# Optimization experiments

Hardware: AMD Instinct MI355X
Metric: run time of the kernel (lower is better)

The kernel has to match this reference:

```python
import jax, jax.numpy as jnp
import numpy as np

N = 100000
E = 800000
D_IN = 128
D_H = 128
D_OUT = 40
L = 16
ALPHA = 0.1
THETA = 0.5
BN_EPS = 1e-5


def setup_inputs() -> dict:
    key = jax.random.key(0)
    ks = jax.random.split(key, 8)
    x = jax.random.normal(ks[0], (N, D_IN), dtype=jnp.float32)
    edge_row = jax.random.randint(ks[1], (E,), 0, N, dtype=jnp.int32)
    edge_col = jax.random.randint(ks[2], (E,), 0, N, dtype=jnp.int32)
    edge_weight = jax.random.uniform(ks[3], (E,), dtype=jnp.float32) / 8.0  # ~normalized adj values
    W_in = jax.random.normal(ks[4], (D_IN, D_H), dtype=jnp.float32) / np.sqrt(D_IN)
    b_in = jnp.zeros((D_H,), jnp.float32)
    conv_W = jax.random.normal(ks[5], (L, D_H, D_H), dtype=jnp.float32) / np.sqrt(D_H)
    bn_gamma = jnp.ones((L, D_H), jnp.float32)
    bn_beta = jnp.zeros((L, D_H), jnp.float32)
    W_out = jax.random.normal(ks[6], (D_H, D_OUT), dtype=jnp.float32) / np.sqrt(D_H)
    b_out = jnp.zeros((D_OUT,), jnp.float32)
    return {"x": x, "edge_weight": edge_weight, "W_in": W_in, "b_in": b_in,
            "conv_W": conv_W, "bn_gamma": bn_gamma, "bn_beta": bn_beta,
            "W_out": W_out, "b_out": b_out,
            "edge_row": edge_row, "edge_col": edge_col}


def reference(x, edge_weight, W_in, b_in, conv_W, bn_gamma, bn_beta, W_out, b_out, edge_row, edge_col):
    # input linear + relu (dropout p=0 -> identity)
    x0 = jax.nn.relu(x @ W_in + b_in)            # [N, D_H]
    # GCN2Conv beta coefficients: log(theta/layer + 1), layer = 1..L
    betas = jnp.log(THETA / jnp.arange(1, L + 1, dtype=jnp.float32) + 1.0)

    def spmm(h):
        # out[i] = sum_{e: row[e]=i} w[e] * h[col[e]]
        msgs = edge_weight[:, None] * h[edge_col]     # [E, D_H]
        return jax.ops.segment_sum(msgs, edge_row, num_segments=N)

    def layer(h, params):
        W, g, bb, beta = params
        a = spmm(h)                                   # propagate
        a = (1.0 - ALPHA) * a + ALPHA * x0            # initial-residual mix
        a = (1.0 - beta) * a + beta * (a @ W)         # shared-weights identity mapping
        mu = jnp.mean(a, axis=0)                      # BatchNorm1d (training stats)
        var = jnp.var(a, axis=0)
        a = (a - mu) * jax.lax.rsqrt(var + BN_EPS) * g + bb
        a = a + h                                     # residual
        return jax.nn.relu(a), None

    xL, _ = jax.lax.scan(layer, x0, (conv_W, bn_gamma, bn_beta, betas))
    return xL @ W_out + b_out                         # [N, D_OUT]
```

## Files before the change

### kernel.cpp

```cpp
#include <hip/hip_runtime.h>
#include <math.h>

#define NN 100000
#define EE 800000
#define DH 128
#define NL 16
#define GEMM_GRID 1563
#define SG_GRID 782
#define NSLOT 32

typedef __bf16 bf16x8 __attribute__((ext_vector_type(8)));
typedef float f32x4 __attribute__((ext_vector_type(4)));

__global__ void k_hist(const int* __restrict__ row, int* __restrict__ cnt) {
    int e = blockIdx.x * 256 + threadIdx.x;
    if (e < EE) atomicAdd(&cnt[row[e]], 1);
}

__global__ void k_scan1(const int* __restrict__ cnt, int* __restrict__ rp, int* __restrict__ part) {
    __shared__ int buf[512];
    int tid = threadIdx.x;
    int i = blockIdx.x * 512 + tid;
    int v = (i < NN) ? cnt[i] : 0;
    buf[tid] = v;
    __syncthreads();
    for (int off = 1; off < 512; off <<= 1) {
        int x = (tid >= off) ? buf[tid - off] : 0;
        __syncthreads();
        buf[tid] += x;
        __syncthreads();
    }
    if (i < NN) rp[i] = buf[tid] - v;
    if (tid == 511) part[blockIdx.x] = buf[511];
}

__global__ void k_scan2(int* __restrict__ part, int nparts) {
    __shared__ int buf[256];
    int tid = threadIdx.x;
    int v = (tid < nparts) ? part[tid] : 0;
    buf[tid] = v;
    __syncthreads();
    for (int off = 1; off < 256; off <<= 1) {
        int x = (tid >= off) ? buf[tid - off] : 0;
        __syncthreads();
        buf[tid] += x;
        __syncthreads();
    }
    if (tid < nparts) part[tid] = buf[tid] - v;
}

__global__ void k_scan3(int* __restrict__ rp, const int* __restrict__ part) {
    int i = blockIdx.x * 512 + threadIdx.x;
    if (i < NN) rp[i] += part[blockIdx.x];
    if (i == 0) rp[NN] = EE;
}

__global__ void k_fill(const int* __restrict__ row, const int* __restrict__ col,
                       const float* __restrict__ w, const int* __restrict__ rp,
                       int* __restrict__ fil, int2* __restrict__ ep) {
    int e = blockIdx.x * 256 + threadIdx.x;
    if (e >= EE) return;
    int r = row[e];
    int pos = rp[r] + atomicAdd(&fil[r], 1);
    ep[pos] = make_int2(col[e], __float_as_int(0.9f * w[e]));
}

__global__ void k_prep_w(const float* __restrict__ convW, const float* __restrict__ Win,
                         __bf16* __restrict__ Bhi, __bf16* __restrict__ Blo) {
    int l = blockIdx.x;
    const float* W;
    float beta, ob;
    if (l < NL) {
        beta = logf(0.5f / (float)(l + 1) + 1.0f);
        ob = 1.0f - beta;
        W = convW + (size_t)l * DH * DH;
    } else {
        beta = 1.0f;
        ob = 0.0f;
        W = Win;
    }
    __bf16* bh = Bhi + (size_t)l * DH * DH;
    __bf16* bl = Blo + (size_t)l * DH * DH;
    for (int i = threadIdx.x; i < DH * DH; i += 256) {
        int k = i >> 7, j = i & 127;
        float v = beta * W[i] + ((k == j) ? ob : 0.f);
        __bf16 hv = (__bf16)v;
        int t = j >> 4, n = j & 15, ks = k >> 5, quad = (k >> 3) & 3, e = k & 7;
        int off = ((t * 4 + ks) * 64 + quad * 16 + n) * 8 + e;
        bh[off] = hv;
        bl[off] = (__bf16)(v - (float)hv);
    }
}

__global__ void k_prep_out(const float* __restrict__ Wout, __bf16* __restrict__ Bhi, __bf16* __restrict__ Blo) {
    for (int i = threadIdx.x; i < DH * 48; i += 256) {
        int k = i / 48, j = i % 48;
        float v = (j < 40) ? Wout[k * 40 + j] : 0.f;
        __bf16 hv = (__bf16)v;
        int t = j >> 4, n = j & 15, ks = k >> 5, quad = (k >> 3) & 3, e = k & 7;
        int off = ((t * 4 + ks) * 64 + quad * 16 + n) * 8 + e;
        Bhi[off] = hv;
        Blo[off] = (__bf16)(v - (float)hv);
    }
}

__device__ inline void split8(const float* p, bf16x8& hi, bf16x8& lo) {
    f32x4 v0 = *(const f32x4*)p;
    f32x4 v1 = *(const f32x4*)(p + 4);
#pragma unroll
    for (int j = 0; j < 4; ++j) {
        __bf16 h0 = (__bf16)v0[j];
        hi[j] = h0;
        lo[j] = (__bf16)(v0[j] - (float)h0);
        __bf16 h1 = (__bf16)v1[j];
        hi[4 + j] = h1;
        lo[4 + j] = (__bf16)(v1[j] - (float)h1);
    }
}

#define MFMA(a, b, c) __builtin_amdgcn_mfma_f32_16x16x32_bf16(a, b, c, 0, 0, 0)

__device__ inline float dec_scale(unsigned int sc4, int ks) {
    return __uint_as_float(((sc4 >> (8 * ks)) & 0xffu) << 23);
}

#define DEC_DW(dw, wsv, a0, a1, a2, a3)                         \
    {                                                           \
        a0 = fmaf(wsv, (float)((dw)&0xffu), a0);                \
        a1 = fmaf(wsv, (float)(((dw) >> 8) & 0xffu), a1);       \
        a2 = fmaf(wsv, (float)(((dw) >> 16) & 0xffu), a2);      \
        a3 = fmaf(wsv, (float)((dw) >> 24), a3);                \
    }

#define EDGE_FMA(S4, W, RA, RB)                                       \
    {                                                                 \
        float _w = (W);                                               \
        float _w0 = _w * dec_scale(S4, 0);                            \
        float _w1 = _w * dec_scale(S4, 1);                            \
        float _w2 = _w * dec_scale(S4, 2);                            \
        float _w3 = _w * dec_scale(S4, 3);                            \
        sw0 += _w0; sw1 += _w1; sw2 += _w2; sw3 += _w3;               \
        DEC_DW((RA).x, _w0, acc[0][0], acc[0][1], acc[0][2], acc[0][3]); \
        DEC_DW((RA).y, _w0, acc[0][4], acc[0][5], acc[0][6], acc[0][7]); \
        DEC_DW((RA).z, _w1, acc[1][0], acc[1][1], acc[1][2], acc[1][3]); \
        DEC_DW((RA).w, _w1, acc[1][4], acc[1][5], acc[1][6], acc[1][7]); \
        DEC_DW((RB).x, _w2, acc[2][0], acc[2][1], acc[2][2], acc[2][3]); \
        DEC_DW((RB).y, _w2, acc[2][4], acc[2][5], acc[2][6], acc[2][7]); \
        DEC_DW((RB).z, _w3, acc[3][0], acc[3][1], acc[3][2], acc[3][3]); \
        DEC_DW((RB).w, _w3, acc[3][4], acc[3][5], acc[3][6], acc[3][7]); \
    }

__global__ void k_cvt8(const __bf16* __restrict__ src, unsigned char* __restrict__ q8,
                       unsigned char* __restrict__ sc) {
    int t = blockIdx.x * 256 + threadIdx.x;
    if (t >= NN * 4) return;
    int node = t >> 2, ks = t & 3;
    const __bf16* p = src + (size_t)node * DH + ks * 32;
    float v[32];
    float mx = 0.f;
#pragma unroll
    for (int i = 0; i < 4; ++i) {
        bf16x8 b = *(const bf16x8*)(p + i * 8);
#pragma unroll
        for (int c = 0; c < 8; ++c) {
            float f = (float)b[c];
            v[i * 8 + c] = f;
            mx = fmaxf(mx, fabsf(f));
        }
    }
    unsigned int em = (__float_as_uint(mx) >> 23) & 0xffu;
    unsigned int eb;
    float sinv;
    if (em < 7) { eb = 0; sinv = 0.f; }
    else { eb = em - 6; sinv = __uint_as_float((254 - eb) << 23); }
    sc[(size_t)node * 4 + ks] = (unsigned char)eb;
    unsigned char* bp = q8 + (size_t)node * 128 + (ks >> 1) * 64 + (ks & 1) * 8;
#pragma unroll
    for (int q = 0; q < 4; ++q) {
        uint2 w;
        w.x = 0; w.y = 0;
#pragma unroll
        for (int c = 0; c < 4; ++c) {
            unsigned int q0 = (unsigned int)rintf(fminf(fmaf(v[q * 8 + c], sinv, 128.f), 255.f));
            unsigned int q1 = (unsigned int)rintf(fminf(fmaf(v[q * 8 + 4 + c], sinv, 128.f), 255.f));
            w.x |= q0 << (8 * c);
            w.y |= q1 << (8 * c);
        }
        *(uint2*)(bp + q * 16) = w;
    }
}

__global__ __launch_bounds__(512, 4) void k_spmm_gemm(const unsigned char* __restrict__ hin8,
                                                      const unsigned char* __restrict__ hinsc,
                                                      const unsigned char* __restrict__ x08,
                                                      const unsigned char* __restrict__ x0sc,
                                                      const int* __restrict__ rp, const int2* __restrict__ ep,
                                                      __bf16* __restrict__ aout,
                                                      const __bf16* __restrict__ Bhi, const __bf16* __restrict__ Blo,
                                                      float* __restrict__ stats32) {
    __shared__ __bf16 Bs[2 * DH * DH];
    __shared__ float red[2][8][DH];
    int tid = threadIdx.x;
    {
        const f32x4* sh = (const f32x4*)Bhi;
        const f32x4* sl = (const f32x4*)Blo;
        f32x4* dh = (f32x4*)Bs;
        f32x4* dl = (f32x4*)(Bs + DH * DH);
#pragma unroll
        for (int i = 0; i < 4; ++i) {
            dh[tid + i * 512] = sh[tid + i * 512];
            dl[tid + i * 512] = sl[tid + i * 512];
        }
    }

    int wave = tid >> 6, lane = tid & 63;
    int n = lane & 15, quad = lane >> 4;
    int r0 = blockIdx.x * 128 + wave * 16;
    int node = r0 + n;
    int nc = (node < NN) ? node : (NN - 1);

    float acc[4][8];
#pragma unroll
    for (int ks = 0; ks < 4; ++ks)
#pragma unroll
        for (int c = 0; c < 8; ++c) acc[ks][c] = 0.f;
    float sw0 = 0.f, sw1 = 0.f, sw2 = 0.f, sw3 = 0.f;

    unsigned xs4 = *(const unsigned*)&x0sc[(size_t)nc * 4];
    const unsigned char* xb = x08 + (size_t)nc * 128 + quad * 16;
    uint4 xa = *(const uint4*)xb;
    uint4 xc = *(const uint4*)(xb + 64);

    int s = 0, e = 0;
    if (node < NN) { s = rp[node]; e = rp[node + 1]; }
    int cnt = e - s;
    int npairs = cnt >> 1;

    const unsigned char* hb = hin8 + quad * 16;

    int2 cP0, cP1, fP0, fP1;
    unsigned cS0, cS1;
    uint4 cA0, cB0, cA1, cB1;
    if (npairs > 0) {
        cP0 = ep[s]; cP1 = ep[s + 1];
        cS0 = *(const unsigned*)&hinsc[(size_t)cP0.x * 4];
        cS1 = *(const unsigned*)&hinsc[(size_t)cP1.x * 4];
        const unsigned char* b0 = hb + (size_t)cP0.x * 128;
        const unsigned char* b1 = hb + (size_t)cP1.x * 128;
        cA0 = *(const uint4*)b0; cB0 = *(const uint4*)(b0 + 64);
        cA1 = *(const uint4*)b1; cB1 = *(const uint4*)(b1 + 64);
        int jf = s + 2; if (jf > EE - 2) jf = EE - 2;
        fP0 = ep[jf]; fP1 = ep[jf + 1];
    }

    EDGE_FMA(xs4, 0.1f, xa, xc);

    int j = s;
    for (int it = 0; it < npairs; ++it) {
        int j2 = j + 4; if (j2 > EE - 2) j2 = EE - 2;
        int2 eN0 = ep[j2], eN1 = ep[j2 + 1];
        unsigned tS0 = *(const unsigned*)&hinsc[(size_t)fP0.x * 4];
        unsigned tS1 = *(const unsigned*)&hinsc[(size_t)fP1.x * 4];
        const unsigned char* b0 = hb + (size_t)fP0.x * 128;
        const unsigned char* b1 = hb + (size_t)fP1.x * 128;
        uint4 tA0 = *(const uint4*)b0, tB0 = *(const uint4*)(b0 + 64);
        uint4 tA1 = *(const uint4*)b1, tB1 = *(const uint4*)(b1 + 64);
        EDGE_FMA(cS0, __int_as_float(cP0.y), cA0, cB0);
        EDGE_FMA(cS1, __int_as_float(cP1.y), cA1, cB1);
        cP0 = fP0; cP1 = fP1; fP0 = eN0; fP1 = eN1;
        cS0 = tS0; cS1 = tS1;
        cA0 = tA0; cB0 = tB0; cA1 = tA1; cB1 = tB1;
        j += 2;
    }
    if (cnt & 1) {
        int2 pe = ep[e - 1];
        unsigned s4 = *(const unsigned*)&hinsc[(size_t)pe.x * 4];
        const unsigned char* bp = hb + (size_t)pe.x * 128;
        uint4 ra = *(const uint4*)bp, rb = *(const uint4*)(bp + 64);
        EDGE_FMA(s4, __int_as_float(pe.y), ra, rb);
    }

    bf16x8 av[4];
    {
        float sws[4] = {sw0, sw1, sw2, sw3};
#pragma unroll
        for (int ks = 0; ks < 4; ++ks)
#pragma unroll
            for (int c = 0; c < 8; ++c)
                av[ks][c] = (__bf16)(acc[ks][c] - 128.0f * sws[ks]);
    }

    __syncthreads();

    f32x4 gacc[8];
#pragma unroll
    for (int t = 0; t < 8; ++t) gacc[t] = (f32x4){0.f, 0.f, 0.f, 0.f};

#pragma unroll
    for (int ks = 0; ks < 4; ++ks) {
#pragma unroll
        for (int t = 0; t < 8; ++t) {
            int base = ((t * 4 + ks) * 64 + lane) * 8;
            bf16x8 bh = *(const bf16x8*)&Bs[base];
            bf16x8 bl = *(const bf16x8*)&Bs[DH * DH + base];
            gacc[t] = MFMA(av[ks], bh, gacc[t]);
            gacc[t] = MFMA(av[ks], bl, gacc[t]);
        }
    }

#pragma unroll
    for (int t = 0; t < 8; ++t) {
        float sm = 0.f, qq = 0.f;
#pragma unroll
        for (int r = 0; r < 4; ++r) {
            int row = r0 + quad * 4 + r;
            float v = gacc[t][r];
            if (row < NN) {
                aout[(size_t)row * DH + t * 16 + n] = (__bf16)v;
                sm += v;
                qq += v * v;
            }
        }
        sm += __shfl_xor(sm, 16); sm += __shfl_xor(sm, 32);
        qq += __shfl_xor(qq, 16); qq += __shfl_xor(qq, 32);
        if (quad == 0) {
            red[0][wave][t * 16 + n] = sm;
            red[1][wave][t * 16 + n] = qq;
        }
    }
    __syncthreads();
    if (tid < 256) {
        int which = tid >> 7, jj = tid & 127;
        float tot = 0.f;
#pragma unroll
        for (int w = 0; w < 8; ++w) tot += red[which][w][jj];
        atomicAdd(&stats32[(size_t)(blockIdx.x & (NSLOT - 1)) * 256 + tid], tot);
    }
}

__global__ __launch_bounds__(256) void k_lin_in(const float* __restrict__ X,
                                                const __bf16* __restrict__ Bhi, const __bf16* __restrict__ Blo,
                                                const float* __restrict__ bin, __bf16* __restrict__ x0) {
    __shared__ __bf16 Bs[2 * DH * DH];
    int tid = threadIdx.x;
    {
        const f32x4* sh = (const f32x4*)Bhi;
        const f32x4* sl = (const f32x4*)Blo;
        f32x4* dh = (f32x4*)Bs;
        f32x4* dl = (f32x4*)(Bs + DH * DH);
#pragma unroll
        for (int i = 0; i < 8; ++i) {
            dh[tid + i * 256] = sh[tid + i * 256];
            dl[tid + i * 256] = sl[tid + i * 256];
        }
    }
    __syncthreads();

    int wave = tid >> 6, lane = tid & 63;
    int n = lane & 15, quad = lane >> 4;
    int r0 = blockIdx.x * 64 + wave * 16;
    int arow = r0 + n;
    if (arow > NN - 1) arow = NN - 1;
    const float* pa = X + (size_t)arow * DH + quad * 8;

    f32x4 acc[8];
#pragma unroll
    for (int t = 0; t < 8; ++t) acc[t] = (f32x4){0.f, 0.f, 0.f, 0.f};

#pragma unroll
    for (int ks = 0; ks < 4; ++ks) {
        bf16x8 ah, al;
        split8(pa + ks * 32, ah, al);
#pragma unroll
        for (int t = 0; t < 8; ++t) {
            int base = ((t * 4 + ks) * 64 + lane) * 8;
            bf16x8 bh = *(const bf16x8*)&Bs[base];
            bf16x8 bl = *(const bf16x8*)&Bs[DH * DH + base];
            acc[t] = MFMA(ah, bh, acc[t]);
            acc[t] = MFMA(al, bh, acc[t]);
            acc[t] = MFMA(ah, bl, acc[t]);
        }
    }

#pragma unroll
    for (int t = 0; t < 8; ++t) {
        float bj = bin[t * 16 + n];
#pragma unroll
        for (int r = 0; r < 4; ++r) {
            int row = r0 + quad * 4 + r;
            if (row < NN) {
                float v = fmaxf(acc[t][r] + bj, 0.f);
                x0[(size_t)row * DH + t * 16 + n] = (__bf16)v;
            }
        }
    }
}

__global__ __launch_bounds__(256) void k_gemm_out(const __bf16* __restrict__ A,
                                                  const __bf16* __restrict__ Bhi, const __bf16* __restrict__ Blo,
                                                  const float* __restrict__ bout, float* __restrict__ out) {
    __shared__ __bf16 Bs[2 * 48 * DH];
    int tid = threadIdx.x;
    {
        const f32x4* sh = (const f32x4*)Bhi;
        const f32x4* sl = (const f32x4*)Blo;
        f32x4* dh = (f32x4*)Bs;
        f32x4* dl = (f32x4*)(Bs + 48 * DH);
#pragma unroll
        for (int i = 0; i < 3; ++i) {
            dh[tid + i * 256] = sh[tid + i * 256];
            dl[tid + i * 256] = sl[tid + i * 256];
        }
    }
    __syncthreads();

    int wave = tid >> 6, lane = tid & 63;
    int n = lane & 15, quad = lane >> 4;
    int r0 = blockIdx.x * 64 + wave * 16;
    int arow = r0 + n;
    if (arow > NN - 1) arow = NN - 1;
    const __bf16* pa = A + (size_t)arow * DH + quad * 8;

    f32x4 acc[3];
#pragma unroll
    for (int t = 0; t < 3; ++t) acc[t] = (f32x4){0.f, 0.f, 0.f, 0.f};

#pragma unroll
    for (int ks = 0; ks < 4; ++ks) {
        bf16x8 av = *(const bf16x8*)(pa + ks * 32);
#pragma unroll
        for (int t = 0; t < 3; ++t) {
            int base = ((t * 4 + ks) * 64 + lane) * 8;
            bf16x8 bh = *(const bf16x8*)&Bs[base];
            bf16x8 bl = *(const bf16x8*)&Bs[48 * DH + base];
            acc[t] = MFMA(av, bh, acc[t]);
            acc[t] = MFMA(av, bl, acc[t]);
        }
    }

#pragma unroll
    for (int t = 0; t < 3; ++t) {
        int j = t * 16 + n;
        float bj = (j < 40) ? bout[j] : 0.f;
#pragma unroll
        for (int r = 0; r < 4; ++r) {
            int row = r0 + quad * 4 + r;
            if (row < NN && j < 40) out[(size_t)row * 40 + j] = acc[t][r] + bj;
        }
    }
}

__global__ __launch_bounds__(256) void k_update(const __bf16* __restrict__ a, const __bf16* __restrict__ hin,
                                                __bf16* __restrict__ hout,
                                                unsigned char* __restrict__ h8, unsigned char* __restrict__ hsc,
                                                const float* __restrict__ stats32,
                                                const float* __restrict__ gamma, const float* __restrict__ bbeta) {
    __shared__ float scb[DH], shb[DH];
    int tid = threadIdx.x;
    if (tid < DH) {
        float s = 0.f, q = 0.f;
#pragma unroll
        for (int sl = 0; sl < NSLOT; ++sl) {
            s += stats32[(size_t)sl * 256 + tid];
            q += stats32[(size_t)sl * 256 + 128 + tid];
        }
        float mu = s * (1.0f / NN);
        float var = q * (1.0f / NN) - mu * mu;
        if (var < 0.f) var = 0.f;
        float sc = gamma[tid] * rsqrtf(var + 1e-5f);
        scb[tid] = sc;
        shb[tid] = bbeta[tid] - mu * sc;
    }
    __syncthreads();

    int idx = blockIdx.x * 256 + tid;
    int sub = idx & 15;
    int j0 = sub * 8;
    bf16x8 av = ((const bf16x8*)a)[idx];
    bf16x8 hv = ((const bf16x8*)hin)[idx];
    bf16x8 o;
    float vv[8];
    float mx = 0.f;
#pragma unroll
    for (int c = 0; c < 8; ++c) {
        int j = j0 + c;
        float v = fmaxf(fmaf((float)av[c], scb[j], shb[j]) + (float)hv[c], 0.f);
        vv[c] = v;
        mx = fmaxf(mx, v);
        o[c] = (__bf16)v;
    }
    ((bf16x8*)hout)[idx] = o;

    mx = fmaxf(mx, __shfl_xor(mx, 1));
    mx = fmaxf(mx, __shfl_xor(mx, 2));
    unsigned int em = (__float_as_uint(mx) >> 23) & 0xffu;
    unsigned int eb;
    float sinv;
    if (em < 7) { eb = 0; sinv = 0.f; }
    else { eb = em - 6; sinv = __uint_as_float((254 - eb) << 23); }
    if ((tid & 3) == 0) hsc[(size_t)(idx >> 4) * 4 + (sub >> 2)] = (unsigned char)eb;
    uint2 pk;
    pk.x = 0; pk.y = 0;
#pragma unroll
    for (int c = 0; c < 4; ++c) {
        unsigned int q0 = (unsigned int)rintf(fminf(fmaf(vv[c], sinv, 128.f), 255.f));
        unsigned int q1 = (unsigned int)rintf(fminf(fmaf(vv[4 + c], sinv, 128.f), 255.f));
        pk.x |= q0 << (8 * c);
        pk.y |= q1 << (8 * c);
    }
    unsigned wpos = ((sub >> 3) & 1) * 64 + (sub & 3) * 16 + ((sub >> 2) & 1) * 8;
    *(uint2*)&h8[(size_t)(idx >> 4) * 128 + wpos] = pk;
}

extern "C" void kernel_launch(void* const* d_in, const int* in_sizes, int n_in,
                              void* d_out, int out_size, void* d_ws, size_t ws_size,
                              hipStream_t stream) {
    const float* x = (const float*)d_in[0];
    const float* ew = (const float*)d_in[1];
    const float* Win = (const float*)d_in[2];
    const float* bin = (const float*)d_in[3];
    const float* convW = (const float*)d_in[4];
    const float* gamma = (const float*)d_in[5];
    const float* bbeta = (const float*)d_in[6];
    const float* Wout = (const float*)d_in[7];
    const float* bout = (const float*)d_in[8];
    const int* erow = (const int*)d_in[9];
    const int* ecol = (const int*)d_in[10];
    float* out = (float*)d_out;

    char* wsp = (char*)d_ws;
    size_t off = 0;
    auto alloc = [&](size_t bytes) -> void* {
        void* p = wsp + off;
        off += (bytes + 255) & ~(size_t)255;
        return p;
    };
    __bf16* x0 = (__bf16*)alloc((size_t)NN * DH * 2);
    __bf16* h = (__bf16*)alloc((size_t)NN * DH * 2);
    __bf16* a = (__bf16*)alloc((size_t)NN * DH * 2);
    unsigned char* x08 = (unsigned char*)alloc((size_t)NN * DH);
    unsigned char* h8 = (unsigned char*)alloc((size_t)NN * DH);
    unsigned char* x0sc = (unsigned char*)alloc((size_t)NN * 4);
    unsigned char* hsc = (unsigned char*)alloc((size_t)NN * 4);
    int* rp = (int*)alloc((NN + 1) * 4);
    size_t zero_bytes = (size_t)NN * 4 + (size_t)NN * 4 + (size_t)NL * NSLOT * 256 * 4;
    int* cnt = (int*)alloc(zero_bytes);
    int* fil = cnt + NN;
    float* stats32 = (float*)(fil + NN);
    int2* ep = (int2*)alloc((size_t)EE * 8);
    int* part = (int*)alloc(256 * 4);
    __bf16* Bhi = (__bf16*)alloc((size_t)(NL + 1) * DH * DH * 2);
    __bf16* Blo = (__bf16*)alloc((size_t)(NL + 1) * DH * DH * 2);
    __bf16* Bohi = (__bf16*)alloc((size_t)DH * 48 * 2);
    __bf16* Bolo = (__bf16*)alloc((size_t)DH * 48 * 2);

    hipMemsetAsync(cnt, 0, zero_bytes, stream);

    k_hist<<<3125, 256, 0, stream>>>(erow, cnt);
    k_scan1<<<196, 512, 0, stream>>>(cnt, rp, part);
    k_scan2<<<1, 256, 0, stream>>>(part, 196);
    k_scan3<<<196, 512, 0, stream>>>(rp, part);
    k_fill<<<3125, 256, 0, stream>>>(erow, ecol, ew, rp, fil, ep);

    k_prep_w<<<NL + 1, 256, 0, stream>>>(convW, Win, Bhi, Blo);
    k_prep_out<<<1, 256, 0, stream>>>(Wout, Bohi, Bolo);

    k_lin_in<<<GEMM_GRID, 256, 0, stream>>>(x, Bhi + (size_t)NL * DH * DH, Blo + (size_t)NL * DH * DH, bin, x0);
    k_cvt8<<<1563, 256, 0, stream>>>(x0, x08, x0sc);

    for (int l = 0; l < NL; ++l) {
        const unsigned char* hin8 = (l == 0) ? x08 : h8;
        const unsigned char* hinsc = (l == 0) ? x0sc : hsc;
        const __bf16* hin = (l == 0) ? x0 : h;
        float* st = stats32 + (size_t)l * NSLOT * 256;
        k_spmm_gemm<<<SG_GRID, 512, 0, stream>>>(hin8, hinsc, x08, x0sc, rp, ep, a,
                                                 Bhi + (size_t)l * DH * DH, Blo + (size_t)l * DH * DH, st);
        k_update<<<6250, 256, 0, stream>>>(a, hin, h, h8, hsc, st, gamma + l * DH, bbeta + l * DH);
    }
    k_gemm_out<<<GEMM_GRID, 256, 0, stream>>>(h, Bohi, Bolo, bout, out);
}
```

Baseline: 1.259 ms.

## Sort nodes by degree for SpMM load balance and window the CSR fill

Measured after the change: 1.174 ms. 6.8% less time.

```diff
diff --git a/kernel.cpp b/kernel.cpp
--- a/kernel.cpp
+++ b/kernel.cpp
@@ -8,6 +8,7 @@
 #define GEMM_GRID 1563
 #define SG_GRID 782
 #define NSLOT 32
+#define WROWS 12500
 
 typedef __bf16 bf16x8 __attribute__((ext_vector_type(8)));
 typedef float f32x4 __attribute__((ext_vector_type(4)));
@@ -55,12 +56,58 @@
     if (i == 0) rp[NN] = EE;
 }
 
+__global__ void k_dhist(const int* __restrict__ cnt, int* __restrict__ dbin) {
+    __shared__ int lb[64];
+    int tid = threadIdx.x;
+    if (tid < 64) lb[tid] = 0;
+    __syncthreads();
+    int i = blockIdx.x * 256 + tid;
+    if (i < NN) {
+        int d = cnt[i];
+        if (d > 63) d = 63;
+        atomicAdd(&lb[63 - d], 1);
+    }
+    __syncthreads();
+    if (tid < 64 && lb[tid]) atomicAdd(&dbin[tid], lb[tid]);
+}
+
+__global__ void k_pscan(const int* __restrict__ dbin, int* __restrict__ dpre) {
+    if (threadIdx.x == 0) {
+        int s = 0;
+        for (int i = 0; i < 64; ++i) { dpre[i] = s; s += dbin[i]; }
+    }
+}
+
+__global__ void k_pscatter(const int* __restrict__ cnt, const int* __restrict__ dpre,
+                           int* __restrict__ dfil, int* __restrict__ perm) {
+    __shared__ int lcnt[64], lbase[64];
+    int tid = threadIdx.x;
+    if (tid < 64) lcnt[tid] = 0;
+    __syncthreads();
+    int i = blockIdx.x * 256 + tid;
+    int b = 0, loc = 0;
+    bool ok = (i < NN);
+    if (ok) {
+        int d = cnt[i];
+        if (d > 63) d = 63;
+        b = 63 - d;
+        loc = atomicAdd(&lcnt[b], 1);
+    }
+    __syncthreads();
+    if (tid < 64 && lcnt[tid]) lbase[tid] = atomicAdd(&dfil[tid], lcnt[tid]);
+    __syncthreads();
+    if (ok) perm[dpre[b] + lbase[b] + loc] = i;
+}
+
 __global__ void k_fill(const int* __restrict__ row, const int* __restrict__ col,
                        const float* __restrict__ w, const int* __restrict__ rp,
                        int* __restrict__ fil, int2* __restrict__ ep) {
-    int e = blockIdx.x * 256 + threadIdx.x;
+    int b = blockIdx.x;
+    int win = b & 7;
+    int e = (b >> 3) * 256 + threadIdx.x;
     if (e >= EE) return;
     int r = row[e];
+    if (r / WROWS != win) return;
     int pos = rp[r] + atomicAdd(&fil[r], 1);
     ep[pos] = make_int2(col[e], __float_as_int(0.9f * w[e]));
 }
@@ -195,6 +242,7 @@
                                                       const unsigned char* __restrict__ x08,
                                                       const unsigned char* __restrict__ x0sc,
                                                       const int* __restrict__ rp, const int2* __restrict__ ep,
+                                                      const int* __restrict__ perm,
                                                       __bf16* __restrict__ aout,
                                                       const __bf16* __restrict__ Bhi, const __bf16* __restrict__ Blo,
                                                       float* __restrict__ stats32) {
@@ -216,8 +264,9 @@
     int wave = tid >> 6, lane = tid & 63;
     int n = lane & 15, quad = lane >> 4;
     int r0 = blockIdx.x * 128 + wave * 16;
-    int node = r0 + n;
-    int nc = (node < NN) ? node : (NN - 1);
+    int idx = r0 + n;
+    int pidx = (idx < NN) ? idx : (NN - 1);
+    int node = perm[pidx];
 
     float acc[4][8];
 #pragma unroll
@@ -226,13 +275,13 @@
         for (int c = 0; c < 8; ++c) acc[ks][c] = 0.f;
     float sw0 = 0.f, sw1 = 0.f, sw2 = 0.f, sw3 = 0.f;
 
-    unsigned xs4 = *(const unsigned*)&x0sc[(size_t)nc * 4];
-    const unsigned char* xb = x08 + (size_t)nc * 128 + quad * 16;
+    unsigned xs4 = *(const unsigned*)&x0sc[(size_t)node * 4];
+    const unsigned char* xb = x08 + (size_t)node * 128 + quad * 16;
     uint4 xa = *(const uint4*)xb;
     uint4 xc = *(const uint4*)(xb + 64);
 
     int s = 0, e = 0;
-    if (node < NN) { s = rp[node]; e = rp[node + 1]; }
+    if (idx < NN) { s = rp[node]; e = rp[node + 1]; }
     int cnt = e - s;
     int npairs = cnt >> 1;
 
@@ -290,6 +339,10 @@
                 av[ks][c] = (__bf16)(acc[ks][c] - 128.0f * sws[ks]);
     }
 
+    int prow[4];
+#pragma unroll
+    for (int r = 0; r < 4; ++r) prow[r] = __shfl(node, quad * 4 + r);
+
     __syncthreads();
 
     f32x4 gacc[8];
@@ -316,7 +369,7 @@
             int row = r0 + quad * 4 + r;
             float v = gacc[t][r];
             if (row < NN) {
-                aout[(size_t)row * DH + t * 16 + n] = (__bf16)v;
+                aout[(size_t)prow[r] * DH + t * 16 + n] = (__bf16)v;
                 sm += v;
                 qq += v * v;
             }
@@ -543,10 +596,14 @@
     unsigned char* x0sc = (unsigned char*)alloc((size_t)NN * 4);
     unsigned char* hsc = (unsigned char*)alloc((size_t)NN * 4);
     int* rp = (int*)alloc((NN + 1) * 4);
-    size_t zero_bytes = (size_t)NN * 4 + (size_t)NN * 4 + (size_t)NL * NSLOT * 256 * 4;
+    int* perm = (int*)alloc((size_t)NN * 4);
+    int* dpre = (int*)alloc(64 * 4);
+    size_t zero_bytes = (size_t)NN * 4 + (size_t)NN * 4 + (size_t)NL * NSLOT * 256 * 4 + 128 * 4;
     int* cnt = (int*)alloc(zero_bytes);
     int* fil = cnt + NN;
     float* stats32 = (float*)(fil + NN);
+    int* dbin = (int*)(stats32 + (size_t)NL * NSLOT * 256);
+    int* dfil = dbin + 64;
     int2* ep = (int2*)alloc((size_t)EE * 8);
     int* part = (int*)alloc(256 * 4);
     __bf16* Bhi = (__bf16*)alloc((size_t)(NL + 1) * DH * DH * 2);
@@ -557,10 +614,13 @@
     hipMemsetAsync(cnt, 0, zero_bytes, stream);
 
     k_hist<<<3125, 256, 0, stream>>>(erow, cnt);
+    k_dhist<<<391, 256, 0, stream>>>(cnt, dbin);
+    k_pscan<<<1, 64, 0, stream>>>(dbin, dpre);
+    k_pscatter<<<391, 256, 0, stream>>>(cnt, dpre, dfil, perm);
     k_scan1<<<196, 512, 0, stream>>>(cnt, rp, part);
     k_scan2<<<1, 256, 0, stream>>>(part, 196);
     k_scan3<<<196, 512, 0, stream>>>(rp, part);
-    k_fill<<<3125, 256, 0, stream>>>(erow, ecol, ew, rp, fil, ep);
+    k_fill<<<25000, 256, 0, stream>>>(erow, ecol, ew, rp, fil, ep);
 
     k_prep_w<<<NL + 1, 256, 0, stream>>>(convW, Win, Bhi, Blo);
     k_prep_out<<<1, 256, 0, stream>>>(Wout, Bohi, Bolo);
@@ -573,7 +633,7 @@
         const unsigned char* hinsc = (l == 0) ? x0sc : hsc;
         const __bf16* hin = (l == 0) ? x0 : h;
         float* st = stats32 + (size_t)l * NSLOT * 256;
-        k_spmm_gemm<<<SG_GRID, 512, 0, stream>>>(hin8, hinsc, x08, x0sc, rp, ep, a,
+        k_spmm_gemm<<<SG_GRID, 512, 0, stream>>>(hin8, hinsc, x08, x0sc, rp, ep, perm, a,
                                                  Bhi + (size_t)l * DH * DH, Blo + (size_t)l * DH * DH, st);
         k_update<<<6250, 256, 0, stream>>>(a, hin, h, h8, hsc, st, gamma + l * DH, bbeta + l * DH);
     }
```
